# Kernel optimization log

Hardware: AMD Instinct MI355X
Metric: run time of the kernel (lower is better)

## Reference

```python
import jax, jax.numpy as jnp
import numpy as np

TEMP = 11.313708498984761  # sqrt(d_k=128)

def setup_inputs() -> dict:
    key = jax.random.key(0)
    ks = jax.random.split(key, 5)
    B, H, T, D = 8, 8, 1024, 128
    shp = (B, H, T, D)
    return {
        "q_time": jax.random.normal(ks[0], shp, dtype=jnp.float32),
        "k_time": jax.random.normal(ks[1], shp, dtype=jnp.float32),
        "q_feature": jax.random.normal(ks[2], shp, dtype=jnp.float32),
        "k_feature": jax.random.normal(ks[3], shp, dtype=jnp.float32),
        "v": jax.random.normal(ks[4], shp, dtype=jnp.float32),
    }

def reference(q_time, k_time, q_feature, k_feature, v):
    # time attention: [B,H,T,T]
    scores_t = jnp.einsum("bhtd,bhsd->bhts", q_time / TEMP, k_time)
    attn_time = jax.nn.softmax(scores_t, axis=-1)
    # feature attention: q_feature^T @ k_feature -> [B,H,D,D]
    scores_f = jnp.einsum("bhtd,bhte->bhde", q_feature / TEMP, k_feature)
    attn_feature = jax.nn.softmax(scores_f, axis=-1)
    # output = attn_time @ v @ attn_feature : [B,H,T,D]
    tv = jnp.einsum("bhts,bhsd->bhtd", attn_time, v)
    output = jnp.einsum("bhtd,bhde->bhte", tv, attn_feature)
    return output, attn_time, attn_feature
```

## Files before the change

### kernel.cpp

```cpp
#include <hip/hip_runtime.h>

typedef __bf16 bf16x8 __attribute__((ext_vector_type(8)));
typedef __bf16 bf16x4 __attribute__((ext_vector_type(4)));
typedef float f32x4 __attribute__((ext_vector_type(4)));

#define T_DIM 1024
#define D_DIM 128
#define NHEAD 64

static constexpr float INV_TEMP = 0.08838834764831845f;
static constexpr size_t OUT_ATTN = (size_t)NHEAD * T_DIM * D_DIM;
static constexpr size_t OUT_AF = OUT_ATTN + (size_t)NHEAD * T_DIM * T_DIM;

#define MFMA16 __builtin_amdgcn_mfma_f32_16x16x32_bf16

__device__ __forceinline__ int swz(int row, int col) {
  return (row << 7) + ((((col >> 3) ^ row) & 15) << 3) + (col & 7);
}

__device__ __forceinline__ bf16x8 ld8(const __bf16* buf, int row, int col) {
  return *reinterpret_cast<const bf16x8*>(&buf[swz(row, col)]);
}

__device__ __forceinline__ void stage_f32_tile_128(const float* __restrict__ src,
                                                   __bf16* dst, int tid, float scale) {
  const float4* s4 = reinterpret_cast<const float4*>(src);
#pragma unroll
  for (int i = 0; i < 16; ++i) {
    int flat = i * 256 + tid;
    int row = flat >> 5;
    int c4 = (flat & 31) << 2;
    float4 vq = s4[flat];
    bf16x4 b;
    b[0] = (__bf16)(vq.x * scale);
    b[1] = (__bf16)(vq.y * scale);
    b[2] = (__bf16)(vq.z * scale);
    b[3] = (__bf16)(vq.w * scale);
    *reinterpret_cast<bf16x4*>(&dst[swz(row, c4)]) = b;
  }
}

__device__ __forceinline__ void stage_wt_tile(const __bf16* __restrict__ src,
                                              __bf16* dst, int tid) {
#pragma unroll
  for (int i = 0; i < 8; ++i) {
    int flat = i * 256 + tid;
    int row = flat >> 4;
    int c8 = (flat & 15) << 3;
    bf16x8 vv = *reinterpret_cast<const bf16x8*>(src + (size_t)row * T_DIM + c8);
    *reinterpret_cast<bf16x8*>(&dst[swz(row, c8)]) = vv;
  }
}

__device__ __forceinline__ void compute_S(const bf16x8 afrag[4][2], const __bf16* bufB,
                                          int l16, int quad, f32x4 sacc[2][8]) {
#pragma unroll
  for (int mt = 0; mt < 2; ++mt)
#pragma unroll
    for (int nt = 0; nt < 8; ++nt)
      sacc[mt][nt] = (f32x4){0.f, 0.f, 0.f, 0.f};
#pragma unroll
  for (int ki = 0; ki < 4; ++ki) {
    bf16x8 bfr[8];
#pragma unroll
    for (int nt = 0; nt < 8; ++nt)
      bfr[nt] = ld8(bufB, nt * 16 + l16, ki * 32 + quad * 8);
#pragma unroll
    for (int nt = 0; nt < 8; ++nt) {
      sacc[0][nt] = MFMA16(afrag[ki][0], bfr[nt], sacc[0][nt], 0, 0, 0);
      sacc[1][nt] = MFMA16(afrag[ki][1], bfr[nt], sacc[1][nt], 0, 0, 0);
    }
  }
}

__global__ __launch_bounds__(256, 2)
void cd_attn_feature(const float* __restrict__ qf, const float* __restrict__ kf,
                     float* __restrict__ out) {
  __shared__ __bf16 qfT[64][40];
  __shared__ __bf16 kfT[128][40];
  const int tid = threadIdx.x;
  const int w = tid >> 6;
  const int lane = tid & 63;
  const int quad = lane >> 4;
  const int l16 = lane & 15;
  const int head = blockIdx.x & 63;
  const int dstart = (blockIdx.x >> 6) << 6;

  const float* __restrict__ qfh = qf + (size_t)head * (T_DIM * D_DIM);
  const float* __restrict__ kfh = kf + (size_t)head * (T_DIM * D_DIM);

  f32x4 acc[8];
#pragma unroll
  for (int nt = 0; nt < 8; ++nt) acc[nt] = (f32x4){0.f, 0.f, 0.f, 0.f};

  for (int tc = 0; tc < T_DIM; tc += 32) {
    __syncthreads();
#pragma unroll
    for (int i = 0; i < 2; ++i) {
      int flat = i * 256 + tid;
      int t = flat >> 4;
      int d4 = (flat & 15) << 2;
      float4 vv = *reinterpret_cast<const float4*>(qfh + (size_t)(tc + t) * D_DIM + dstart + d4);
      qfT[d4 + 0][t] = (__bf16)vv.x;
      qfT[d4 + 1][t] = (__bf16)vv.y;
      qfT[d4 + 2][t] = (__bf16)vv.z;
      qfT[d4 + 3][t] = (__bf16)vv.w;
    }
#pragma unroll
    for (int i = 0; i < 4; ++i) {
      int flat = i * 256 + tid;
      int t = flat >> 5;
      int e4 = (flat & 31) << 2;
      float4 vv = *reinterpret_cast<const float4*>(kfh + (size_t)(tc + t) * D_DIM + e4);
      kfT[e4 + 0][t] = (__bf16)vv.x;
      kfT[e4 + 1][t] = (__bf16)vv.y;
      kfT[e4 + 2][t] = (__bf16)vv.z;
      kfT[e4 + 3][t] = (__bf16)vv.w;
    }
    __syncthreads();
    bf16x8 a = *reinterpret_cast<const bf16x8*>(&qfT[w * 16 + l16][quad * 8]);
#pragma unroll
    for (int nt = 0; nt < 8; ++nt) {
      bf16x8 b = *reinterpret_cast<const bf16x8*>(&kfT[nt * 16 + l16][quad * 8]);
      acc[nt] = MFMA16(a, b, acc[nt], 0, 0, 0);
    }
  }

  float p[8][4];
  float rsum[4] = {0.f, 0.f, 0.f, 0.f};
#pragma unroll
  for (int nt = 0; nt < 8; ++nt)
#pragma unroll
    for (int r = 0; r < 4; ++r) {
      p[nt][r] = __expf(acc[nt][r] * INV_TEMP);
      rsum[r] += p[nt][r];
    }
#pragma unroll
  for (int off = 1; off < 16; off <<= 1)
#pragma unroll
    for (int r = 0; r < 4; ++r)
      rsum[r] += __shfl_xor(rsum[r], off, 64);
#pragma unroll
  for (int r = 0; r < 4; ++r) rsum[r] = 1.0f / rsum[r];

  float* __restrict__ afh = out + OUT_AF + (size_t)head * (D_DIM * D_DIM);
#pragma unroll
  for (int nt = 0; nt < 8; ++nt)
#pragma unroll
    for (int r = 0; r < 4; ++r)
      afh[(size_t)(dstart + w * 16 + quad * 4 + r) * D_DIM + nt * 16 + l16] = p[nt][r] * rsum[r];
}

__global__ __launch_bounds__(256, 2)
void cd_attn_w(const float* __restrict__ v, const float* __restrict__ out_ro,
               __bf16* __restrict__ wt) {
  __shared__ __bf16 vt[128 * 128];
  __shared__ __bf16 aft[128 * 128];
  const int tid = threadIdx.x;
  const int w = tid >> 6;
  const int lane = tid & 63;
  const int quad = lane >> 4;
  const int l16 = lane & 15;
  const int head = blockIdx.x & 63;
  const int t0 = (blockIdx.x >> 6) << 7;

  const float* __restrict__ vh = v + (size_t)head * (T_DIM * D_DIM);
  const float* __restrict__ afh = out_ro + OUT_AF + (size_t)head * (D_DIM * D_DIM);

#pragma unroll
  for (int i = 0; i < 16; ++i) {
    int flat = i * 256 + tid;
    int d = flat >> 5;
    int e4 = (flat & 31) << 2;
    float4 vv = *reinterpret_cast<const float4*>(afh + (size_t)d * D_DIM + e4);
    aft[swz(e4 + 0, d)] = (__bf16)vv.x;
    aft[swz(e4 + 1, d)] = (__bf16)vv.y;
    aft[swz(e4 + 2, d)] = (__bf16)vv.z;
    aft[swz(e4 + 3, d)] = (__bf16)vv.w;
  }
  stage_f32_tile_128(vh + (size_t)t0 * D_DIM, vt, tid, 1.0f);
  __syncthreads();

  f32x4 acc[2][8];
#pragma unroll
  for (int mt = 0; mt < 2; ++mt)
#pragma unroll
    for (int nt = 0; nt < 8; ++nt) acc[mt][nt] = (f32x4){0.f, 0.f, 0.f, 0.f};

#pragma unroll
  for (int ki = 0; ki < 4; ++ki) {
    bf16x8 a0 = ld8(vt, w * 32 + l16, ki * 32 + quad * 8);
    bf16x8 a1 = ld8(vt, w * 32 + 16 + l16, ki * 32 + quad * 8);
#pragma unroll
    for (int nt = 0; nt < 8; ++nt) {
      bf16x8 b = ld8(aft, nt * 16 + l16, ki * 32 + quad * 8);
      acc[0][nt] = MFMA16(a0, b, acc[0][nt], 0, 0, 0);
      acc[1][nt] = MFMA16(a1, b, acc[1][nt], 0, 0, 0);
    }
  }

  __bf16* __restrict__ wth = wt + (size_t)head * (D_DIM * T_DIM);
#pragma unroll
  for (int mt = 0; mt < 2; ++mt)
#pragma unroll
    for (int nt = 0; nt < 8; ++nt) {
      int e = nt * 16 + l16;
      int tt = t0 + w * 32 + mt * 16 + quad * 4;
      bf16x4 pk;
      pk[0] = (__bf16)acc[mt][nt][0];
      pk[1] = (__bf16)acc[mt][nt][1];
      pk[2] = (__bf16)acc[mt][nt][2];
      pk[3] = (__bf16)acc[mt][nt][3];
      *reinterpret_cast<bf16x4*>(&wth[(size_t)e * T_DIM + tt]) = pk;
    }
}

__global__ __launch_bounds__(256, 2)
void cd_attn_time(const float* __restrict__ qt, const float* __restrict__ kt,
                  const __bf16* __restrict__ wt, float* __restrict__ out) {
  __shared__ __bf16 bufB[128 * 128];
  __shared__ __bf16 bufP[128 * 128];
  const int tid = threadIdx.x;
  const int w = tid >> 6;
  const int lane = tid & 63;
  const int quad = lane >> 4;
  const int l16 = lane & 15;
  const int head = blockIdx.x & 63;
  const int t0 = (blockIdx.x >> 6) << 7;

  const float* __restrict__ qth = qt + (size_t)head * (T_DIM * D_DIM);
  const float* __restrict__ kth = kt + (size_t)head * (T_DIM * D_DIM);
  const __bf16* __restrict__ wth = wt + (size_t)head * (D_DIM * T_DIM);
  float* __restrict__ attn_out = out + OUT_ATTN + (size_t)head * ((size_t)T_DIM * T_DIM);
  float* __restrict__ o_out = out + (size_t)head * (T_DIM * D_DIM);

  stage_f32_tile_128(qth + (size_t)t0 * D_DIM, bufB, tid, INV_TEMP);
  __syncthreads();
  bf16x8 afrag[4][2];
#pragma unroll
  for (int ki = 0; ki < 4; ++ki) {
    afrag[ki][0] = ld8(bufB, w * 32 + l16, ki * 32 + quad * 8);
    afrag[ki][1] = ld8(bufB, w * 32 + 16 + l16, ki * 32 + quad * 8);
  }

  float rs[2][4] = {{0.f, 0.f, 0.f, 0.f}, {0.f, 0.f, 0.f, 0.f}};
  for (int j = 0; j < 8; ++j) {
    __syncthreads();
    stage_f32_tile_128(kth + (size_t)(j * 128) * D_DIM, bufB, tid, 1.0f);
    __syncthreads();
    f32x4 sacc[2][8];
    compute_S(afrag, bufB, l16, quad, sacc);
#pragma unroll
    for (int mt = 0; mt < 2; ++mt)
#pragma unroll
      for (int nt = 0; nt < 8; ++nt)
#pragma unroll
        for (int r = 0; r < 4; ++r)
          rs[mt][r] += __expf(sacc[mt][nt][r]);
  }
#pragma unroll
  for (int off = 1; off < 16; off <<= 1)
#pragma unroll
    for (int mt = 0; mt < 2; ++mt)
#pragma unroll
      for (int r = 0; r < 4; ++r)
        rs[mt][r] += __shfl_xor(rs[mt][r], off, 64);
  float invl[2][4];
#pragma unroll
  for (int mt = 0; mt < 2; ++mt)
#pragma unroll
    for (int r = 0; r < 4; ++r)
      invl[mt][r] = 1.0f / rs[mt][r];

  f32x4 uacc[2][8];
#pragma unroll
  for (int mt = 0; mt < 2; ++mt)
#pragma unroll
    for (int nt = 0; nt < 8; ++nt) uacc[mt][nt] = (f32x4){0.f, 0.f, 0.f, 0.f};

  for (int j = 0; j < 8; ++j) {
    __syncthreads();
    stage_f32_tile_128(kth + (size_t)(j * 128) * D_DIM, bufB, tid, 1.0f);
    __syncthreads();
    f32x4 sacc[2][8];
    compute_S(afrag, bufB, l16, quad, sacc);
    __syncthreads();
    stage_wt_tile(wth + j * 128, bufB, tid);
#pragma unroll
    for (int mt = 0; mt < 2; ++mt)
#pragma unroll
      for (int nt = 0; nt < 8; ++nt)
#pragma unroll
        for (int r = 0; r < 4; ++r) {
          float p = __expf(sacc[mt][nt][r]) * invl[mt][r];
          bufP[swz(w * 32 + mt * 16 + quad * 4 + r, nt * 16 + l16)] = (__bf16)p;
        }
    __syncthreads();
    const int s0 = j * 128;
#pragma unroll
    for (int i = 0; i < 8; ++i) {
      int row = i * 16 + (tid >> 4);
      int pc = tid & 15;
      bf16x8 pv = *reinterpret_cast<const bf16x8*>(&bufP[(row << 7) + (pc << 3)]);
      int col = ((pc ^ row) & 15) << 3;
      float4 o1, o2;
      o1.x = (float)pv[0]; o1.y = (float)pv[1]; o1.z = (float)pv[2]; o1.w = (float)pv[3];
      o2.x = (float)pv[4]; o2.y = (float)pv[5]; o2.z = (float)pv[6]; o2.w = (float)pv[7];
      float4* dstp = reinterpret_cast<float4*>(attn_out + (size_t)(t0 + row) * T_DIM + s0 + col);
      dstp[0] = o1;
      dstp[1] = o2;
    }
#pragma unroll
    for (int ki = 0; ki < 4; ++ki) {
      bf16x8 aP0 = ld8(bufP, w * 32 + l16, ki * 32 + quad * 8);
      bf16x8 aP1 = ld8(bufP, w * 32 + 16 + l16, ki * 32 + quad * 8);
#pragma unroll
      for (int nt = 0; nt < 8; ++nt) {
        bf16x8 bW = ld8(bufB, nt * 16 + l16, ki * 32 + quad * 8);
        uacc[0][nt] = MFMA16(aP0, bW, uacc[0][nt], 0, 0, 0);
        uacc[1][nt] = MFMA16(aP1, bW, uacc[1][nt], 0, 0, 0);
      }
    }
  }

#pragma unroll
  for (int mt = 0; mt < 2; ++mt)
#pragma unroll
    for (int nt = 0; nt < 8; ++nt)
#pragma unroll
      for (int r = 0; r < 4; ++r)
        o_out[(size_t)(t0 + w * 32 + mt * 16 + quad * 4 + r) * D_DIM + nt * 16 + l16] =
            uacc[mt][nt][r];
}

extern "C" void kernel_launch(void* const* d_in, const int* in_sizes, int n_in,
                              void* d_out, int out_size, void* d_ws, size_t ws_size,
                              hipStream_t stream) {
  (void)in_sizes; (void)n_in; (void)out_size; (void)ws_size;
  const float* q_time    = (const float*)d_in[0];
  const float* k_time    = (const float*)d_in[1];
  const float* q_feature = (const float*)d_in[2];
  const float* k_feature = (const float*)d_in[3];
  const float* v         = (const float*)d_in[4];
  float* out = (float*)d_out;
  __bf16* wt = (__bf16*)d_ws;

  cd_attn_feature<<<128, 256, 0, stream>>>(q_feature, k_feature, out);
  cd_attn_w<<<512, 256, 0, stream>>>(v, out, wt);
  cd_attn_time<<<512, 256, 0, stream>>>(q_time, k_time, wt, out);
}
```

Before: 746.1 us.

## Pre-convert Q/K to bf16 and pipeline time-attention with async LDS loads

Adds a prep kernel that converts q_time (pre-scaled) and k_time to bf16 in the workspace. A new time-attention kernel then streams K and W tiles straight into LDS with global_load_lds, double-buffered across the softmax-sum pass and the output pass. The P tile is written out through LDS as coalesced float4 rows. The W-producing kernel also transposes through LDS so its global stores are coalesced 16-byte writes. The costs are an extra kernel launch, extra workspace traffic for the bf16 copies, and a fallback path that depends on the workspace size.

```diff
diff --git a/kernel.cpp b/kernel.cpp
--- a/kernel.cpp
+++ b/kernel.cpp
@@ -52,6 +52,28 @@
   }
 }
 
+__device__ __forceinline__ void cp16_async(const void* g, void* l) {
+  typedef __attribute__((address_space(1))) unsigned int gu32;
+  typedef __attribute__((address_space(3))) unsigned int lu32;
+  __builtin_amdgcn_global_load_lds((gu32*)g, (lu32*)l, 16, 0, 0);
+}
+
+__device__ __forceinline__ void stage_async_tile(const __bf16* __restrict__ gbase,
+                                                 int row_stride_elems,
+                                                 __bf16* lbuf, int tid) {
+  const int w = tid >> 6;
+  const int lane = tid & 63;
+#pragma unroll
+  for (int i = 0; i < 8; ++i) {
+    int seg = i * 4 + w;
+    int row = seg * 4 + (lane >> 4);
+    int c = ((lane & 15) ^ row) & 15;
+    const void* src = (const void*)(gbase + (size_t)row * row_stride_elems + c * 8);
+    void* dst = (void*)(lbuf + seg * 512);
+    cp16_async(src, dst);
+  }
+}
+
 __device__ __forceinline__ void compute_S(const bf16x8 afrag[4][2], const __bf16* bufB,
                                           int l16, int quad, f32x4 sacc[2][8]) {
 #pragma unroll
@@ -71,6 +93,29 @@
       sacc[1][nt] = MFMA16(afrag[ki][1], bfr[nt], sacc[1][nt], 0, 0, 0);
     }
   }
+}
+
+__global__ __launch_bounds__(256)
+void cd_prep(const float* __restrict__ qt, const float* __restrict__ kt,
+             __bf16* __restrict__ qtb, __bf16* __restrict__ ktb) {
+  const size_t NC = (size_t)NHEAD * T_DIM * D_DIM / 8;
+  size_t i = (size_t)blockIdx.x * 256 + threadIdx.x;
+  const float4* s4;
+  __bf16* d;
+  float sc;
+  if (i < NC) {
+    s4 = reinterpret_cast<const float4*>(qt); d = qtb; sc = INV_TEMP;
+  } else {
+    s4 = reinterpret_cast<const float4*>(kt); d = ktb; sc = 1.0f; i -= NC;
+  }
+  float4 a = s4[i * 2];
+  float4 b = s4[i * 2 + 1];
+  bf16x8 o;
+  o[0] = (__bf16)(a.x * sc); o[1] = (__bf16)(a.y * sc);
+  o[2] = (__bf16)(a.z * sc); o[3] = (__bf16)(a.w * sc);
+  o[4] = (__bf16)(b.x * sc); o[5] = (__bf16)(b.y * sc);
+  o[6] = (__bf16)(b.z * sc); o[7] = (__bf16)(b.w * sc);
+  *reinterpret_cast<bf16x8*>(d + i * 8) = o;
 }
 
 __global__ __launch_bounds__(256, 2)
@@ -199,20 +244,157 @@
     }
   }
 
+  __syncthreads();
+#pragma unroll
+  for (int mt = 0; mt < 2; ++mt)
+#pragma unroll
+    for (int nt = 0; nt < 8; ++nt)
+#pragma unroll
+      for (int r = 0; r < 4; ++r)
+        aft[swz(nt * 16 + l16, w * 32 + mt * 16 + quad * 4 + r)] = (__bf16)acc[mt][nt][r];
+  __syncthreads();
+
   __bf16* __restrict__ wth = wt + (size_t)head * (D_DIM * T_DIM);
 #pragma unroll
-  for (int mt = 0; mt < 2; ++mt)
-#pragma unroll
-    for (int nt = 0; nt < 8; ++nt) {
-      int e = nt * 16 + l16;
-      int tt = t0 + w * 32 + mt * 16 + quad * 4;
-      bf16x4 pk;
-      pk[0] = (__bf16)acc[mt][nt][0];
-      pk[1] = (__bf16)acc[mt][nt][1];
-      pk[2] = (__bf16)acc[mt][nt][2];
-      pk[3] = (__bf16)acc[mt][nt][3];
-      *reinterpret_cast<bf16x4*>(&wth[(size_t)e * T_DIM + tt]) = pk;
-    }
+  for (int i = 0; i < 8; ++i) {
+    int row = i * 16 + (tid >> 4);
+    int pc = tid & 15;
+    bf16x8 vv = *reinterpret_cast<const bf16x8*>(&aft[(row << 7) + (pc << 3)]);
+    int col = ((pc ^ row) & 15) << 3;
+    *reinterpret_cast<bf16x8*>(&wth[(size_t)row * T_DIM + t0 + col]) = vv;
+  }
+}
+
+__global__ __launch_bounds__(256, 2)
+void cd_attn_time_v2(const __bf16* __restrict__ qtb, const __bf16* __restrict__ ktb,
+                     const __bf16* __restrict__ wt, float* __restrict__ out) {
+  __shared__ __bf16 buf0[128 * 128];
+  __shared__ __bf16 buf1[128 * 128];
+  const int tid = threadIdx.x;
+  const int w = tid >> 6;
+  const int lane = tid & 63;
+  const int quad = lane >> 4;
+  const int l16 = lane & 15;
+  const int head = blockIdx.x & 63;
+  const int t0 = (blockIdx.x >> 6) << 7;
+
+  const __bf16* __restrict__ qth = qtb + (size_t)head * (T_DIM * D_DIM);
+  const __bf16* __restrict__ kth = ktb + (size_t)head * (T_DIM * D_DIM);
+  const __bf16* __restrict__ wth = wt + (size_t)head * (D_DIM * T_DIM);
+  float* __restrict__ attn_out = out + OUT_ATTN + (size_t)head * ((size_t)T_DIM * T_DIM);
+  float* __restrict__ o_out = out + (size_t)head * (T_DIM * D_DIM);
+
+  stage_async_tile(kth, D_DIM, buf0, tid);
+  bf16x8 afrag[4][2];
+#pragma unroll
+  for (int ki = 0; ki < 4; ++ki) {
+#pragma unroll
+    for (int mt = 0; mt < 2; ++mt)
+      afrag[ki][mt] = *reinterpret_cast<const bf16x8*>(
+          qth + (size_t)(t0 + w * 32 + mt * 16 + l16) * D_DIM + ki * 32 + quad * 8);
+  }
+
+  float rs[2][4] = {{0.f, 0.f, 0.f, 0.f}, {0.f, 0.f, 0.f, 0.f}};
+  for (int j = 0; j < 8; ++j) {
+    if (j < 7) {
+      stage_async_tile(kth + (size_t)(j + 1) * (128 * D_DIM), D_DIM,
+                       (j & 1) ? buf0 : buf1, tid);
+      asm volatile("s_waitcnt vmcnt(8)" ::: "memory");
+    } else {
+      asm volatile("s_waitcnt vmcnt(0)" ::: "memory");
+    }
+    __builtin_amdgcn_s_barrier();
+    f32x4 sacc[2][8];
+    compute_S(afrag, (j & 1) ? buf1 : buf0, l16, quad, sacc);
+#pragma unroll
+    for (int mt = 0; mt < 2; ++mt)
+#pragma unroll
+      for (int nt = 0; nt < 8; ++nt)
+#pragma unroll
+        for (int r = 0; r < 4; ++r)
+          rs[mt][r] += __expf(sacc[mt][nt][r]);
+    asm volatile("s_waitcnt lgkmcnt(0)" ::: "memory");
+    __builtin_amdgcn_s_barrier();
+  }
+#pragma unroll
+  for (int off = 1; off < 16; off <<= 1)
+#pragma unroll
+    for (int mt = 0; mt < 2; ++mt)
+#pragma unroll
+      for (int r = 0; r < 4; ++r)
+        rs[mt][r] += __shfl_xor(rs[mt][r], off, 64);
+  float invl[2][4];
+#pragma unroll
+  for (int mt = 0; mt < 2; ++mt)
+#pragma unroll
+    for (int r = 0; r < 4; ++r)
+      invl[mt][r] = 1.0f / rs[mt][r];
+
+  f32x4 uacc[2][8];
+#pragma unroll
+  for (int mt = 0; mt < 2; ++mt)
+#pragma unroll
+    for (int nt = 0; nt < 8; ++nt) uacc[mt][nt] = (f32x4){0.f, 0.f, 0.f, 0.f};
+
+  stage_async_tile(kth, D_DIM, buf0, tid);
+  stage_async_tile(wth, T_DIM, buf1, tid);
+  for (int j = 0; j < 8; ++j) {
+    asm volatile("s_waitcnt vmcnt(8)" ::: "memory");
+    __builtin_amdgcn_s_barrier();
+    f32x4 sacc[2][8];
+    compute_S(afrag, buf0, l16, quad, sacc);
+    asm volatile("s_waitcnt lgkmcnt(0)" ::: "memory");
+    __builtin_amdgcn_s_barrier();
+#pragma unroll
+    for (int mt = 0; mt < 2; ++mt)
+#pragma unroll
+      for (int nt = 0; nt < 8; ++nt)
+#pragma unroll
+        for (int r = 0; r < 4; ++r)
+          buf0[swz(w * 32 + mt * 16 + quad * 4 + r, nt * 16 + l16)] =
+              (__bf16)(__expf(sacc[mt][nt][r]) * invl[mt][r]);
+    __syncthreads();
+#pragma unroll
+    for (int ki = 0; ki < 4; ++ki) {
+      bf16x8 aP0 = ld8(buf0, w * 32 + l16, ki * 32 + quad * 8);
+      bf16x8 aP1 = ld8(buf0, w * 32 + 16 + l16, ki * 32 + quad * 8);
+#pragma unroll
+      for (int nt = 0; nt < 8; ++nt) {
+        bf16x8 bW = ld8(buf1, nt * 16 + l16, ki * 32 + quad * 8);
+        uacc[0][nt] = MFMA16(aP0, bW, uacc[0][nt], 0, 0, 0);
+        uacc[1][nt] = MFMA16(aP1, bW, uacc[1][nt], 0, 0, 0);
+      }
+    }
+    const int s0 = j * 128;
+#pragma unroll
+    for (int i = 0; i < 8; ++i) {
+      int row = i * 16 + (tid >> 4);
+      int pc = tid & 15;
+      bf16x8 pv = *reinterpret_cast<const bf16x8*>(&buf0[(row << 7) + (pc << 3)]);
+      int col = ((pc ^ row) & 15) << 3;
+      float4 o1, o2;
+      o1.x = (float)pv[0]; o1.y = (float)pv[1]; o1.z = (float)pv[2]; o1.w = (float)pv[3];
+      o2.x = (float)pv[4]; o2.y = (float)pv[5]; o2.z = (float)pv[6]; o2.w = (float)pv[7];
+      float4* dstp = reinterpret_cast<float4*>(attn_out + (size_t)(t0 + row) * T_DIM + s0 + col);
+      dstp[0] = o1;
+      dstp[1] = o2;
+    }
+    asm volatile("s_waitcnt lgkmcnt(0)" ::: "memory");
+    __builtin_amdgcn_s_barrier();
+    if (j < 7) {
+      stage_async_tile(kth + (size_t)(j + 1) * (128 * D_DIM), D_DIM, buf0, tid);
+      stage_async_tile(wth + (size_t)(j + 1) * 128, T_DIM, buf1, tid);
+    }
+  }
+
+#pragma unroll
+  for (int mt = 0; mt < 2; ++mt)
+#pragma unroll
+    for (int nt = 0; nt < 8; ++nt)
+#pragma unroll
+      for (int r = 0; r < 4; ++r)
+        o_out[(size_t)(t0 + w * 32 + mt * 16 + quad * 4 + r) * D_DIM + nt * 16 + l16] =
+            uacc[mt][nt][r];
 }
 
 __global__ __launch_bounds__(256, 2)
@@ -336,7 +518,7 @@
 extern "C" void kernel_launch(void* const* d_in, const int* in_sizes, int n_in,
                               void* d_out, int out_size, void* d_ws, size_t ws_size,
                               hipStream_t stream) {
-  (void)in_sizes; (void)n_in; (void)out_size; (void)ws_size;
+  (void)in_sizes; (void)n_in; (void)out_size;
   const float* q_time    = (const float*)d_in[0];
   const float* k_time    = (const float*)d_in[1];
   const float* q_feature = (const float*)d_in[2];
@@ -345,7 +527,19 @@
   float* out = (float*)d_out;
   __bf16* wt = (__bf16*)d_ws;
 
-  cd_attn_feature<<<128, 256, 0, stream>>>(q_feature, k_feature, out);
-  cd_attn_w<<<512, 256, 0, stream>>>(v, out, wt);
-  cd_attn_time<<<512, 256, 0, stream>>>(q_time, k_time, wt, out);
-}
+  const size_t NELEM = (size_t)NHEAD * T_DIM * D_DIM;
+  const size_t WS_NEED = NELEM * 2 * 3;
+
+  if (ws_size >= WS_NEED) {
+    __bf16* qtb = wt + NELEM;
+    __bf16* ktb = qtb + NELEM;
+    cd_prep<<<8192, 256, 0, stream>>>(q_time, k_time, qtb, ktb);
+    cd_attn_feature<<<128, 256, 0, stream>>>(q_feature, k_feature, out);
+    cd_attn_w<<<512, 256, 0, stream>>>(v, out, wt);
+    cd_attn_time_v2<<<512, 256, 0, stream>>>(qtb, ktb, wt, out);
+  } else {
+    cd_attn_feature<<<128, 256, 0, stream>>>(q_feature, k_feature, out);
+    cd_attn_w<<<512, 256, 0, stream>>>(v, out, wt);
+    cd_attn_time<<<512, 256, 0, stream>>>(q_time, k_time, wt, out);
+  }
+}
```

Result: no change. 738.3 us (-1.0%).
